# Kernel optimization log

Hardware: AMD Instinct MI355X
Metric: run time of the kernel (lower is better)

## Reference

```python
import jax, jax.numpy as jnp
import numpy as np

L, D, F, H = 4, 1024, 2048, 8
DH = D // H
EPS = 1e-5


def setup_inputs() -> dict:
    key = jax.random.key(0)
    ks = jax.random.split(key, 8)
    B, S = 4, 1024
    sd = 1.0 / np.sqrt(D)
    sf = 1.0 / np.sqrt(F)
    return {
        "X": jax.random.normal(ks[0], (B, S, D), jnp.float32),
        "Wq": jax.random.normal(ks[1], (L, D, D), jnp.float32) * sd,
        "Wk": jax.random.normal(ks[2], (L, D, D), jnp.float32) * sd,
        "Wv": jax.random.normal(ks[3], (L, D, D), jnp.float32) * sd,
        "Wg": jax.random.normal(ks[4], (L, D, D), jnp.float32) * sd,
        "Wo": jax.random.normal(ks[5], (L, D, D), jnp.float32) * sd,
        "W1": jax.random.normal(ks[6], (L, D, F), jnp.float32) * sd,
        "W2": jax.random.normal(ks[7], (L, F, D), jnp.float32) * sf,
        "ln_scale": jnp.ones((D,), jnp.float32),
        "ln_bias": jnp.zeros((D,), jnp.float32),
        "gn_scale": jnp.ones((L, D), jnp.float32),
        "gn_bias": jnp.zeros((L, D), jnp.float32),
    }


def _layer_norm(x, scale, bias):
    mu = x.mean(-1, keepdims=True)
    var = x.var(-1, keepdims=True)
    return (x - mu) * jax.lax.rsqrt(var + EPS) * scale + bias


def _rotate(x, cos, sin):
    # x: (B,S,H,DH); cos/sin: (1,S,1,DH//2); rotary pairs (even, odd)
    x1, x2 = x[..., 0::2], x[..., 1::2]
    r1 = x1 * cos - x2 * sin
    r2 = x1 * sin + x2 * cos
    return jnp.stack([r1, r2], axis=-1).reshape(x.shape)


def _decay_matrix(S):
    # D[h,n,m] = gamma_h^(n-m) for n>=m else 0
    gammas = 1.0 - jnp.exp(jnp.linspace(np.log(1 / 32), np.log(1 / 512), H)).astype(jnp.float32)
    n = jnp.arange(S)
    diff = (n[:, None] - n[None, :]).astype(jnp.float32)
    pw = jnp.exp(jnp.clip(diff, 0.0)[None] * jnp.log(gammas)[:, None, None])
    return jnp.where(diff[None] >= 0, pw, 0.0)  # (H,S,S)


def _retention(x, Wq, Wk, Wv, Wg, Wo, gn_s, gn_b, Dm, cos, sin):
    B, S, _ = x.shape
    Q = (x @ Wq).reshape(B, S, H, DH)
    K = (x @ Wk).reshape(B, S, H, DH)
    V = (x @ Wv).reshape(B, S, H, DH)
    Q = _rotate(Q, cos, sin)
    K = _rotate(K, cos, -sin)  # conjugate phase
    att = jnp.einsum('bnhd,bmhd->bhnm', Q, K) * Dm  # (B,H,S,S)
    Y = jnp.einsum('bhnm,bmhd->bnhd', att, V)
    # group norm: normalize each head's output per token
    mu = Y.mean(-1, keepdims=True)
    var = Y.var(-1, keepdims=True)
    Y = (Y - mu) * jax.lax.rsqrt(var + EPS)
    Y = Y.reshape(B, S, D) * gn_s + gn_b
    G = jax.nn.swish(x @ Wg)
    return (G * Y) @ Wo


def reference(X, Wq, Wk, Wv, Wg, Wo, W1, W2, ln_scale, ln_bias, gn_scale, gn_bias):
    B, S, _ = X.shape
    pos = jnp.arange(S, dtype=jnp.float32)
    inv_freq = 1.0 / (10000.0 ** (jnp.arange(0, DH, 2, dtype=jnp.float32) / DH))
    ang = pos[:, None] * inv_freq[None, :]  # (S, DH//2)
    cos = jnp.cos(ang)[None, :, None, :]
    sin = jnp.sin(ang)[None, :, None, :]
    Dm = _decay_matrix(S)
    for i in range(L):
        Yr = _retention(_layer_norm(X, ln_scale, ln_bias), Wq[i], Wk[i], Wv[i],
                        Wg[i], Wo[i], gn_scale[i], gn_bias[i], Dm, cos, sin) + X
        X = jax.nn.gelu(_layer_norm(Yr, ln_scale, ln_bias) @ W1[i]) @ W2[i] + Yr
    return X
```

## Files before the change

kernel.cpp:

```cpp
#include <hip/hip_runtime.h>
#include <hip/hip_bf16.h>
#include <cmath>

#define LAYERS 4
#define Bb 4
#define Ss 1024
#define Dd 1024
#define Ff 2048
#define Hh 8
#define DHd 128
#define Mm (Bb * Ss)
#define EPSf 1e-5f
#define LDQ 4096

typedef __attribute__((ext_vector_type(8))) short short8v;
typedef __attribute__((ext_vector_type(4))) float f32x4;
typedef __attribute__((ext_vector_type(4))) unsigned int u32x4;

__device__ __forceinline__ float swish_f(float x) { return x / (1.f + expf(-x)); }
__device__ __forceinline__ float gelu_f(float x) {
  return 0.5f * x * (1.f + tanhf(0.7978845608028654f * (x + 0.044715f * x * x * x)));
}
__device__ __forceinline__ unsigned short f2bfu(float f) {
  __hip_bfloat16 h = __float2bfloat16(f);
  return __builtin_bit_cast(unsigned short, h);
}
__device__ __forceinline__ float bfu2f(unsigned short u) {
  unsigned v = ((unsigned)u) << 16;
  return __builtin_bit_cast(float, v);
}
__device__ __forceinline__ void gl_lds16(const void* g, void* l) {
  __builtin_amdgcn_global_load_lds((__attribute__((address_space(1))) void*)g,
                                   (__attribute__((address_space(3))) void*)l, 16, 0, 0);
}
__device__ __forceinline__ f32x4 mfma16(short8v a, short8v b, f32x4 c) {
  return __builtin_amdgcn_mfma_f32_16x16x32_bf16(a, b, c, 0, 0, 0);
}

__global__ __launch_bounds__(256) void ln_bf16_kernel(const float* __restrict__ x,
                                                      short* __restrict__ outb,
                                                      const float* __restrict__ sc,
                                                      const float* __restrict__ bi) {
  const int row = blockIdx.x;
  const int t = threadIdx.x;
  const float4 v = *(const float4*)(x + (size_t)row * Dd + t * 4);
  float s = v.x + v.y + v.z + v.w;
  float s2 = v.x * v.x + v.y * v.y + v.z * v.z + v.w * v.w;
#pragma unroll
  for (int o = 32; o > 0; o >>= 1) { s += __shfl_down(s, o); s2 += __shfl_down(s2, o); }
  __shared__ float ps[4], ps2[4];
  if ((t & 63) == 0) { ps[t >> 6] = s; ps2[t >> 6] = s2; }
  __syncthreads();
  s = ps[0] + ps[1] + ps[2] + ps[3];
  s2 = ps2[0] + ps2[1] + ps2[2] + ps2[3];
  const float mu = s * (1.f / Dd);
  const float var = s2 * (1.f / Dd) - mu * mu;
  const float rstd = rsqrtf(var + EPSf);
  const float4 g = *(const float4*)(sc + t * 4);
  const float4 b = *(const float4*)(bi + t * 4);
  const float o0 = (v.x - mu) * rstd * g.x + b.x;
  const float o1 = (v.y - mu) * rstd * g.y + b.y;
  const float o2 = (v.z - mu) * rstd * g.z + b.z;
  const float o3 = (v.w - mu) * rstd * g.w + b.w;
  unsigned p0 = (unsigned)f2bfu(o0) | ((unsigned)f2bfu(o1) << 16);
  unsigned p1 = (unsigned)f2bfu(o2) | ((unsigned)f2bfu(o3) << 16);
  uint2 pk; pk.x = p0; pk.y = p1;
  *(uint2*)(outb + (size_t)row * Dd + t * 4) = pk;
}

__global__ void rope_table_kernel(float* __restrict__ ct, float* __restrict__ st) {
  const int i = blockIdx.x * 256 + threadIdx.x;
  const int s = i >> 6, f = i & 63;
  const float inv = powf(10000.f, -(float)f / 64.f);
  const float a = (float)s * inv;
  ct[i] = cosf(a);
  st[i] = sinf(a);
}

__global__ void rope_ip_kernel(short* __restrict__ QK, const float* __restrict__ ct,
                               const float* __restrict__ st) {
  const int idx = blockIdx.x * 256 + threadIdx.x;
  const int f = idx & 63;
  const int h = (idx >> 6) & 7;
  const int r = idx >> 9;
  const int s = r & (Ss - 1);
  const float c = ct[(s << 6) + f], sn = st[(s << 6) + f];
  const size_t qo = (size_t)r * LDQ + h * DHd + 2 * f;
  const unsigned qp = *(const unsigned*)(QK + qo);
  const unsigned kp = *(const unsigned*)(QK + qo + 1024);
  const float qx = bfu2f((unsigned short)(qp & 0xffff)), qy = bfu2f((unsigned short)(qp >> 16));
  const float kx = bfu2f((unsigned short)(kp & 0xffff)), ky = bfu2f((unsigned short)(kp >> 16));
  const unsigned qn = (unsigned)f2bfu(qx * c - qy * sn) | ((unsigned)f2bfu(qx * sn + qy * c) << 16);
  const unsigned kn = (unsigned)f2bfu(kx * c + ky * sn) | ((unsigned)f2bfu(-kx * sn + ky * c) << 16);
  *(unsigned*)(QK + qo) = qn;
  *(unsigned*)(QK + qo + 1024) = kn;
}

__global__ __launch_bounds__(256) void wtrans4_kernel(const float* __restrict__ W0,
                                                      const float* __restrict__ W1,
                                                      const float* __restrict__ W2,
                                                      const float* __restrict__ W3,
                                                      short* __restrict__ Wt) {
  __shared__ float tile[32][33];
  const int t = threadIdx.x;
  const int n0 = blockIdx.x * 32, k0 = blockIdx.y * 32;
  const int which = n0 >> 10;
  const float* W = (which == 0) ? W0 : (which == 1) ? W1 : (which == 2) ? W2 : W3;
  const int nl = n0 & 1023;
  const int tc = t & 31, tr8 = t >> 5;
#pragma unroll
  for (int i = 0; i < 4; ++i) {
    const int r = tr8 + i * 8;
    tile[r][tc] = W[(size_t)(k0 + r) * 1024 + nl + tc];
  }
  __syncthreads();
#pragma unroll
  for (int i = 0; i < 4; ++i) {
    const int r = tr8 + i * 8;
    Wt[(size_t)(n0 + r) * 1024 + k0 + tc] = (short)f2bfu(tile[tc][r]);
  }
}

__global__ __launch_bounds__(256) void wtrans1_kernel(const float* __restrict__ W,
                                                      short* __restrict__ Wt, int K, int N) {
  __shared__ float tile[32][33];
  const int t = threadIdx.x;
  const int n0 = blockIdx.x * 32, k0 = blockIdx.y * 32;
  const int tc = t & 31, tr8 = t >> 5;
#pragma unroll
  for (int i = 0; i < 4; ++i) {
    const int r = tr8 + i * 8;
    tile[r][tc] = W[(size_t)(k0 + r) * N + n0 + tc];
  }
  __syncthreads();
#pragma unroll
  for (int i = 0; i < 4; ++i) {
    const int r = tr8 + i * 8;
    Wt[(size_t)(n0 + r) * K + k0 + tc] = (short)f2bfu(tile[tc][r]);
  }
}

__global__ __launch_bounds__(256) void vtrans16_kernel(const short* __restrict__ Vb,
                                                       short* __restrict__ Vt) {
  __shared__ short tile[32][33];
  const int t = threadIdx.x;
  const int s0 = blockIdx.x * 32, d0 = blockIdx.y * 32, bh = blockIdx.z;
  const int bb = bh >> 3, h = bh & 7;
  const int tc = t & 31, tr8 = t >> 5;
#pragma unroll
  for (int i = 0; i < 4; ++i) {
    const int r = tr8 + i * 8;
    tile[r][tc] = Vb[(size_t)(bb * Ss + s0 + r) * LDQ + 2048 + h * DHd + d0 + tc];
  }
  __syncthreads();
#pragma unroll
  for (int i = 0; i < 4; ++i) {
    const int r = tr8 + i * 8;
    Vt[(size_t)(bh * DHd + d0 + r) * Ss + s0 + tc] = tile[tc][r];
  }
}

template <int EPI>
__global__ __launch_bounds__(512, 2) void gemm10(const short* __restrict__ A,
                                                 const short* __restrict__ Bt,
                                                 float* __restrict__ Cf,
                                                 short* __restrict__ Cb,
                                                 const float* __restrict__ Res,
                                                 int N, int K, int ldc) {
  __shared__ __align__(16) short As[2][2][128 * 64];
  __shared__ __align__(16) short Bs[2][2][128 * 64];
  const int t = threadIdx.x;
  const int w = t >> 6, l = t & 63;
  const int lq = l >> 4, lr = l & 15;
  const int wr = w >> 2, wc = w & 3;
  const int bhalf = wc >> 1, brow0 = (wc & 1) * 64;
  const int nwg = gridDim.x * gridDim.y;
  const int bid0 = blockIdx.x + blockIdx.y * gridDim.x;
  const int lgid = (bid0 & 7) * (nwg >> 3) + (bid0 >> 3);
  const int bx = lgid % gridDim.x, by = lgid / gridDim.x;
  const int row0 = by * 256, col0 = bx * 256;
  const int NT = K >> 6;

  f32x4 acc[8][4] = {};
  short8v a[4][2], b[4][2];

  auto stageA = [&](int kt, int hf) {
    const int db = kt & 1;
#pragma unroll
    for (int i = 0; i < 2; ++i) {
      const int c = t + i * 512;
      const int row = c >> 3, slot = c & 7;
      gl_lds16(A + (size_t)(row0 + hf * 128 + row) * K + kt * 64 + ((slot ^ (row & 7)) << 3),
               &As[db][hf][c * 8]);
    }
  };
  auto stageB = [&](int kt, int hf) {
    const int db = kt & 1;
#pragma unroll
    for (int i = 0; i < 2; ++i) {
      const int c = t + i * 512;
      const int row = c >> 3, slot = c & 7;
      gl_lds16(Bt + (size_t)(col0 + hf * 128 + row) * K + kt * 64 + ((slot ^ (row & 7)) << 3),
               &Bs[db][hf][c * 8]);
    }
  };
  auto rdA = [&](int db, int m, int ks) -> short8v {
    const int row = m * 16 + lr;
    return *(const short8v*)&As[db][wr][row * 64 + (((ks << 2) + lq) ^ (row & 7)) * 8];
  };
  auto rdB = [&](int db, int n, int ks) -> short8v {
    const int row = brow0 + n * 16 + lr;
    return *(const short8v*)&Bs[db][bhalf][row * 64 + (((ks << 2) + lq) ^ (row & 7)) * 8];
  };

  stageA(0, 0); stageA(0, 1); stageB(0, 0); stageB(0, 1);
  if (NT > 1) { stageB(1, 0); stageB(1, 1); }
  if (NT > 1) { asm volatile("s_waitcnt vmcnt(4)" ::: "memory"); }
  else        { asm volatile("s_waitcnt vmcnt(0)" ::: "memory"); }
  asm volatile("s_barrier" ::: "memory");

  for (int kt = 0; kt < NT; ++kt) {
    const int db = kt & 1;
#pragma unroll
    for (int m = 0; m < 4; ++m) { a[m][0] = rdA(db, m, 0); a[m][1] = rdA(db, m, 1); }
#pragma unroll
    for (int n = 0; n < 2; ++n) { b[n][0] = rdB(db, n, 0); b[n][1] = rdB(db, n, 1); }
    if (kt + 1 < NT) stageA(kt + 1, 0);
    __builtin_amdgcn_s_setprio(1);
#pragma unroll
    for (int m = 0; m < 4; ++m)
#pragma unroll
      for (int n = 0; n < 2; ++n) {
        acc[m][n] = mfma16(a[m][0], b[n][0], acc[m][n]);
        acc[m][n] = mfma16(a[m][1], b[n][1], acc[m][n]);
      }
    __builtin_amdgcn_s_setprio(0);
    asm volatile("s_barrier" ::: "memory");
#pragma unroll
    for (int n = 2; n < 4; ++n) { b[n][0] = rdB(db, n, 0); b[n][1] = rdB(db, n, 1); }
    if (kt + 1 < NT) stageA(kt + 1, 1);
    __builtin_amdgcn_s_setprio(1);
#pragma unroll
    for (int m = 0; m < 4; ++m)
#pragma unroll
      for (int n = 2; n < 4; ++n) {
        acc[m][n] = mfma16(a[m][0], b[n][0], acc[m][n]);
        acc[m][n] = mfma16(a[m][1], b[n][1], acc[m][n]);
      }
    __builtin_amdgcn_s_setprio(0);
    asm volatile("s_barrier" ::: "memory");
#pragma unroll
    for (int m = 0; m < 4; ++m) { a[m][0] = rdA(db, m + 4, 0); a[m][1] = rdA(db, m + 4, 1); }
    if (kt + 2 < NT) stageB(kt + 2, 0);
    __builtin_amdgcn_s_setprio(1);
#pragma unroll
    for (int m = 0; m < 4; ++m)
#pragma unroll
      for (int n = 0; n < 2; ++n) {
        acc[m + 4][n] = mfma16(a[m][0], b[n][0], acc[m + 4][n]);
        acc[m + 4][n] = mfma16(a[m][1], b[n][1], acc[m + 4][n]);
      }
    __builtin_amdgcn_s_setprio(0);
    asm volatile("s_barrier" ::: "memory");
    if (kt + 2 < NT) stageB(kt + 2, 1);
    __builtin_amdgcn_s_setprio(1);
#pragma unroll
    for (int m = 0; m < 4; ++m)
#pragma unroll
      for (int n = 2; n < 4; ++n) {
        acc[m + 4][n] = mfma16(a[m][0], b[n][0], acc[m + 4][n]);
        acc[m + 4][n] = mfma16(a[m][1], b[n][1], acc[m + 4][n]);
      }
    __builtin_amdgcn_s_setprio(0);
    if (kt + 2 < NT) { asm volatile("s_waitcnt vmcnt(4)" ::: "memory"); }
    else             { asm volatile("s_waitcnt vmcnt(0)" ::: "memory"); }
    asm volatile("s_barrier" ::: "memory");
  }

#pragma unroll
  for (int m = 0; m < 8; ++m) {
#pragma unroll
    for (int n = 0; n < 4; ++n) {
#pragma unroll
      for (int r = 0; r < 4; ++r) {
        const int row = row0 + wr * 128 + m * 16 + lq * 4 + r;
        const int col = col0 + wc * 64 + n * 16 + lr;
        const size_t o = (size_t)row * ldc + col;
        float v = acc[m][n][r];
        if (EPI == 0) Cb[o] = (short)f2bfu(v);
        else if (EPI == 1) Cf[o] = v + Res[o];
        else Cb[o] = (short)f2bfu(gelu_f(v));
      }
    }
  }
}

template <int BM, int BN, int EPI>
__global__ __launch_bounds__(256) void gemm7(const short* __restrict__ A,
                                             const short* __restrict__ Bt,
                                             float* __restrict__ Cf,
                                             short* __restrict__ Cb,
                                             const float* __restrict__ Res,
                                             int N, int K, int ldc) {
  constexpr int NTHR = 256;
  constexpr int WM = BM / 2, WN = BN / 2;
  constexpr int MR = WM / 16, NR = WN / 16;
  constexpr int LA = (BM * 4) / NTHR, LB = (BN * 4) / NTHR;
  __shared__ __align__(16) short As[2][BM * 32];
  __shared__ __align__(16) short Bs[2][BN * 32];
  const int t = threadIdx.x;
  const int w = t >> 6, l = t & 63;
  const int lq = l >> 4, lr = l & 15;
  const int wr = w >> 1, wc = w & 1;
  const int nwg = gridDim.x * gridDim.y;
  const int bid0 = blockIdx.x + blockIdx.y * gridDim.x;
  const int lgid = (bid0 & 7) * (nwg >> 3) + (bid0 >> 3);
  const int bx = lgid % gridDim.x, by = lgid / gridDim.x;
  const int row0 = by * BM, col0 = bx * BN;
  f32x4 acc[MR][NR] = {};
  const int NTK = K >> 5;

  auto stage = [&](int tile, int buf) {
    const int k0 = tile << 5;
#pragma unroll
    for (int i = 0; i < LA; ++i) {
      const int c = t + i * NTHR;
      const int row = c >> 2, sc = c & 3;
      gl_lds16(A + (size_t)(row0 + row) * K + k0 + ((sc ^ ((row >> 1) & 3)) << 3),
               &As[buf][c * 8]);
    }
#pragma unroll
    for (int i = 0; i < LB; ++i) {
      const int c = t + i * NTHR;
      const int row = c >> 2, sc = c & 3;
      gl_lds16(Bt + (size_t)(col0 + row) * K + k0 + ((sc ^ ((row >> 1) & 3)) << 3),
               &Bs[buf][c * 8]);
    }
  };

  stage(0, 0);
  int cur = 0;
  for (int tt = 0; tt < NTK; ++tt) {
    __syncthreads();
    if (tt + 1 < NTK) stage(tt + 1, cur ^ 1);
    short8v a[MR], b[NR];
#pragma unroll
    for (int m = 0; m < MR; ++m) {
      const int row = wr * WM + m * 16 + lr;
      a[m] = *(const short8v*)&As[cur][row * 32 + ((lq ^ ((row >> 1) & 3)) << 3)];
    }
#pragma unroll
    for (int n = 0; n < NR; ++n) {
      const int col = wc * WN + n * 16 + lr;
      b[n] = *(const short8v*)&Bs[cur][col * 32 + ((lq ^ ((col >> 1) & 3)) << 3)];
    }
    __builtin_amdgcn_s_setprio(1);
#pragma unroll
    for (int m = 0; m < MR; ++m)
#pragma unroll
      for (int n = 0; n < NR; ++n) acc[m][n] = mfma16(a[m], b[n], acc[m][n]);
    __builtin_amdgcn_s_setprio(0);
    cur ^= 1;
  }

#pragma unroll
  for (int m = 0; m < MR; ++m) {
#pragma unroll
    for (int n = 0; n < NR; ++n) {
#pragma unroll
      for (int r = 0; r < 4; ++r) {
        const int row = row0 + wr * WM + m * 16 + lq * 4 + r;
        const int col = col0 + wc * WN + n * 16 + lr;
        const size_t o = (size_t)row * ldc + col;
        float v = acc[m][n][r];
        if (EPI == 0) Cb[o] = (short)f2bfu(v);
        else if (EPI == 1) Cf[o] = v + Res[o];
        else Cb[o] = (short)f2bfu(gelu_f(v));
      }
    }
  }
}

__global__ __launch_bounds__(256) void ret4_kernel(const short* __restrict__ QKb,
                                                   const short* __restrict__ Vt,
                                                   float* __restrict__ Y0,
                                                   float* __restrict__ Y1) {
  __shared__ __align__(16) short Ks[2][64 * 128];
  __shared__ __align__(16) short Vs[2][128 * 64];
  const int t = threadIdx.x, w = t >> 6, l = t & 63;
  const int lq = l >> 4, lr = l & 15;
  const int u = blockIdx.x;
  const int lgid = (u & 7) * 64 + (u >> 3);
  const int half = lgid >> 8;
  const int rest = lgid & 255;
  const int bh = rest >> 3, j = rest & 7;
  const int qb = half ? j : 7 - j;
  const int b = bh >> 3, h = bh & 7;
  const int q0 = qb * 128;
  const float lstep = (logf(1.f / 512.f) - logf(1.f / 32.f)) * (1.f / 7.f);
  const float gamma = 1.f - expf(logf(1.f / 32.f) + (float)h * lstep);
  const float l2g = logf(gamma) * 1.44269504f;
  const short* Qp = QKb;
  const short* Kp = QKb + 1024;

  short8v qf[2][4];
#pragma unroll
  for (int qn = 0; qn < 2; ++qn)
#pragma unroll
    for (int ks = 0; ks < 4; ++ks)
      qf[qn][ks] = *(const short8v*)(Qp + (size_t)(b * Ss + q0 + w * 32 + qn * 16 + lr) * LDQ +
                                     h * DHd + ks * 32 + lq * 8);

  float cmf[4], csr[4];
#pragma unroll
  for (int mf = 0; mf < 4; ++mf) cmf[mf] = exp2f(l2g * (float)(-16 * mf));
#pragma unroll
  for (int r = 0; r < 4; ++r) csr[r] = exp2f(l2g * (float)(63 - 4 * lq - r));

  f32x4 yacc[2][8] = {};
  const int nt = 2 * qb + 2;
  const int sb = ((lq & 1) * 2) * 16 + lr;

  auto stageKV = [&](int m0, int buf) {
#pragma unroll
    for (int i = 0; i < 4; ++i) {
      const int c = (w * 4 + i) * 64 + l;
      const int row = c >> 4, slot = c & 15;
      gl_lds16(Kp + (size_t)(b * Ss + m0 + row) * LDQ + h * DHd + ((slot ^ (row & 7)) * 8),
               &Ks[buf][(w * 4 + i) * 512]);
    }
#pragma unroll
    for (int i = 0; i < 4; ++i) {
      const int c = (w * 4 + i) * 64 + l;
      const int row = c >> 3, slot = c & 7;
      gl_lds16(Vt + (size_t)(bh * DHd + row) * Ss + m0 + ((slot ^ (row & 7)) * 8),
               &Vs[buf][(w * 4 + i) * 512]);
    }
  };

  stageKV(half * 64, 0);
  __syncthreads();
  int cur = 0;
  for (int tt = half; tt < nt; tt += 2) {
    const int m0 = tt * 64;
    if (tt + 2 < nt) stageKV((tt + 2) * 64, cur ^ 1);

    f32x4 st[4][2] = {};
    __builtin_amdgcn_s_setprio(1);
#pragma unroll
    for (int mf = 0; mf < 4; ++mf) {
      const int row = mf * 16 + lr;
#pragma unroll
      for (int ks = 0; ks < 4; ++ks) {
        short8v kf = *(const short8v*)&Ks[cur][row * 128 + (((4 * ks + lq) ^ (row & 7)) * 8)];
        st[mf][0] = mfma16(kf, qf[0][ks], st[mf][0]);
        st[mf][1] = mfma16(kf, qf[1][ks], st[mf][1]);
      }
    }
    __builtin_amdgcn_s_setprio(0);
    float rs[2];
#pragma unroll
    for (int qn = 0; qn < 2; ++qn)
      rs[qn] = exp2f(l2g * (float)(q0 + w * 32 + qn * 16 + lr - m0 - 63));
#pragma unroll
    for (int mf = 0; mf < 4; ++mf)
#pragma unroll
      for (int qn = 0; qn < 2; ++qn)
#pragma unroll
        for (int r = 0; r < 4; ++r) {
          const int qg = q0 + w * 32 + qn * 16 + lr;
          const int kvg = m0 + mf * 16 + lq * 4 + r;
          const float wgt = (qg >= kvg) ? rs[qn] * cmf[mf] * csr[r] : 0.f;
          st[mf][qn][r] *= wgt;
        }
    unsigned pk[4][2][2];
#pragma unroll
    for (int mf = 0; mf < 4; ++mf)
#pragma unroll
      for (int qn = 0; qn < 2; ++qn)
#pragma unroll
        for (int p = 0; p < 2; ++p)
          pk[mf][qn][p] = (unsigned)f2bfu(st[mf][qn][2 * p]) |
                          ((unsigned)f2bfu(st[mf][qn][2 * p + 1]) << 16);
    short8v afr[2][2];
#pragma unroll
    for (int qn = 0; qn < 2; ++qn)
#pragma unroll
      for (int ks2 = 0; ks2 < 2; ++ks2) {
        u32x4 wd;
#pragma unroll
        for (int wj = 0; wj < 4; ++wj) {
          const int src = sb + (wj >> 1) * 16;
          const unsigned v0 = __shfl(pk[2 * ks2 + 0][qn][wj & 1], src);
          const unsigned v1 = __shfl(pk[2 * ks2 + 1][qn][wj & 1], src);
          wd[wj] = (lq >= 2) ? v1 : v0;
        }
        afr[qn][ks2] = __builtin_bit_cast(short8v, wd);
      }
    __builtin_amdgcn_s_setprio(1);
#pragma unroll
    for (int nd = 0; nd < 8; ++nd) {
      const int row = nd * 16 + lr;
#pragma unroll
      for (int ks2 = 0; ks2 < 2; ++ks2) {
        short8v vf = *(const short8v*)&Vs[cur][row * 64 + (((4 * ks2 + lq) ^ (row & 7)) * 8)];
        yacc[0][nd] = mfma16(afr[0][ks2], vf, yacc[0][nd]);
        yacc[1][nd] = mfma16(afr[1][ks2], vf, yacc[1][nd]);
      }
    }
    __builtin_amdgcn_s_setprio(0);
    __syncthreads();
    cur ^= 1;
  }
  float* Y = half ? Y1 : Y0;
#pragma unroll
  for (int qn = 0; qn < 2; ++qn)
#pragma unroll
    for (int r = 0; r < 4; ++r) {
      const int q = q0 + w * 32 + qn * 16 + lq * 4 + r;
#pragma unroll
      for (int nd = 0; nd < 8; ++nd)
        Y[(size_t)(b * Ss + q) * Dd + h * DHd + nd * 16 + lr] = yacc[qn][nd][r];
    }
}

__global__ __launch_bounds__(256) void gate_kernel(const float* __restrict__ Y0,
                                                   const float* __restrict__ Y1,
                                                   const short* __restrict__ Graw,
                                                   short* __restrict__ Gb,
                                                   const float* __restrict__ gs,
                                                   const float* __restrict__ gb) {
  const int lane = threadIdx.x & 63;
  const int rowh = blockIdx.x * 4 + (threadIdx.x >> 6);
  const int h = rowh & 7;
  const int row = rowh >> 3;
  const size_t ybase = (size_t)row * Dd + (size_t)h * DHd + lane * 2;
  float2 a = *(const float2*)(Y0 + ybase);
  const float2 c = *(const float2*)(Y1 + ybase);
  a.x += c.x; a.y += c.y;
  float s = a.x + a.y, s2 = a.x * a.x + a.y * a.y;
#pragma unroll
  for (int o = 32; o > 0; o >>= 1) { s += __shfl_down(s, o); s2 += __shfl_down(s2, o); }
  s = __shfl(s, 0);
  s2 = __shfl(s2, 0);
  const float mu = s * (1.f / DHd);
  const float rstd = rsqrtf(s2 * (1.f / DHd) - mu * mu + EPSf);
  const int d = h * DHd + lane * 2;
  const float2 g = *(const float2*)(gs + d);
  const float2 bbv = *(const float2*)(gb + d);
  const float y0 = (a.x - mu) * rstd * g.x + bbv.x;
  const float y1 = (a.y - mu) * rstd * g.y + bbv.y;
  const unsigned gr = *(const unsigned*)(Graw + (size_t)row * LDQ + 3072 + h * DHd + lane * 2);
  const float gx = bfu2f((unsigned short)(gr & 0xffff));
  const float gy = bfu2f((unsigned short)(gr >> 16));
  const unsigned o01 = (unsigned)f2bfu(swish_f(gx) * y0) |
                       ((unsigned)f2bfu(swish_f(gy) * y1) << 16);
  *(unsigned*)(Gb + ybase) = o01;
}

extern "C" void kernel_launch(void* const* d_in, const int* in_sizes, int n_in,
                              void* d_out, int out_size, void* d_ws, size_t ws_size,
                              hipStream_t stream) {
  const float* X = (const float*)d_in[0];
  const float* Wq = (const float*)d_in[1];
  const float* Wk = (const float*)d_in[2];
  const float* Wv = (const float*)d_in[3];
  const float* Wg = (const float*)d_in[4];
  const float* Wo = (const float*)d_in[5];
  const float* W1 = (const float*)d_in[6];
  const float* W2 = (const float*)d_in[7];
  const float* lns = (const float*)d_in[8];
  const float* lnb = (const float*)d_in[9];
  const float* gns = (const float*)d_in[10];
  const float* gnb = (const float*)d_in[11];
  float* out = (float*)d_out;

  char* W = (char*)d_ws;
  const size_t MB = 1u << 20;
  float* Abuf  = (float*)(W);
  short* Xnb   = (short*)(W + 16 * MB);
  short* QKVGb = (short*)(W + 24 * MB);
  float* Y0    = (float*)(W + 56 * MB);
  float* Y1    = (float*)(W + 72 * MB);
  short* Vtb   = (short*)(W + 88 * MB);
  short* Gb    = (short*)(W + 96 * MB);
  short* Wqkvgt= (short*)(W + 104 * MB);
  short* Wot   = (short*)(W + 112 * MB);
  short* W1t   = (short*)(W + 114 * MB);
  short* W2t   = (short*)(W + 118 * MB);
  float* ct    = (float*)(W + 122 * MB);
  float* st    = ct + Ss * 64;
  short* Hb = QKVGb;

  hipMemcpyAsync(Abuf, X, (size_t)Mm * Dd * sizeof(float), hipMemcpyDeviceToDevice, stream);
  rope_table_kernel<<<(Ss * 64) / 256, 256, 0, stream>>>(ct, st);

  for (int l = 0; l < LAYERS; ++l) {
    const size_t DD = (size_t)Dd * Dd;
    wtrans4_kernel<<<dim3(128, 32), 256, 0, stream>>>(Wq + l * DD, Wk + l * DD, Wv + l * DD,
                                                      Wg + l * DD, Wqkvgt);
    wtrans1_kernel<<<dim3(32, 32), 256, 0, stream>>>(Wo + l * DD, Wot, Dd, Dd);
    wtrans1_kernel<<<dim3(64, 32), 256, 0, stream>>>(W1 + (size_t)l * Dd * Ff, W1t, Dd, Ff);
    wtrans1_kernel<<<dim3(32, 64), 256, 0, stream>>>(W2 + (size_t)l * Ff * Dd, W2t, Ff, Dd);

    ln_bf16_kernel<<<Mm, 256, 0, stream>>>(Abuf, Xnb, lns, lnb);
    gemm10<0><<<dim3(16, 16), 512, 0, stream>>>(Xnb, Wqkvgt, nullptr, QKVGb,
                                                nullptr, 4096, Dd, LDQ);
    rope_ip_kernel<<<(Bb * Ss * Hh * 64) / 256, 256, 0, stream>>>(QKVGb, ct, st);
    vtrans16_kernel<<<dim3(Ss / 32, DHd / 32, Bb * Hh), 256, 0, stream>>>(QKVGb, Vtb);
    ret4_kernel<<<512, 256, 0, stream>>>(QKVGb, Vtb, Y0, Y1);
    gate_kernel<<<(Mm * Hh) / 4, 256, 0, stream>>>(Y0, Y1, QKVGb, Gb,
                                                   gns + (size_t)l * Dd, gnb + (size_t)l * Dd);
    gemm7<128, 64, 1><<<dim3(16, 32), 256, 0, stream>>>(Gb, Wot, Abuf, nullptr, Abuf,
                                                        Dd, Dd, Dd);
    ln_bf16_kernel<<<Mm, 256, 0, stream>>>(Abuf, Xnb, lns, lnb);
    gemm7<128, 64, 2><<<dim3(32, 32), 256, 0, stream>>>(Xnb, W1t, nullptr, Hb, nullptr,
                                                        Ff, Dd, Ff);
    float* dst = (l == LAYERS - 1) ? out : Abuf;
    gemm7<64, 64, 1><<<dim3(16, 64), 256, 0, stream>>>(Hb, W2t, dst, nullptr, Abuf,
                                                       Dd, Ff, Dd);
  }
}
```

Measured before the change: 826.1 us.

## Add 256x128 triple-buffered GEMM kernel for the FFN up-projection

Adds a new gemm11 kernel with 256x128 tiles, 512 threads, a three-stage LDS pipeline with split A staging, and a grouped workgroup-to-tile remapping. It replaces gemm7<128,64> for the W1 GEMM with fused GELU. The larger tile raises arithmetic intensity and reuse per block, and the remap is meant to improve L2 locality. In exchange the grid is only 256 workgroups, which could limit occupancy on a chip with many CUs, and LDS use is high (144KB).

```diff
diff --git a/kernel.cpp b/kernel.cpp
--- a/kernel.cpp
+++ b/kernel.cpp
@@ -285,6 +285,113 @@
       for (int r = 0; r < 4; ++r) {
         const int row = row0 + wr * 128 + m * 16 + lq * 4 + r;
         const int col = col0 + wc * 64 + n * 16 + lr;
+        const size_t o = (size_t)row * ldc + col;
+        float v = acc[m][n][r];
+        if (EPI == 0) Cb[o] = (short)f2bfu(v);
+        else if (EPI == 1) Cf[o] = v + Res[o];
+        else Cb[o] = (short)f2bfu(gelu_f(v));
+      }
+    }
+  }
+}
+
+template <int EPI>
+__global__ __launch_bounds__(512) void gemm11(const short* __restrict__ A,
+                                              const short* __restrict__ Bt,
+                                              float* __restrict__ Cf,
+                                              short* __restrict__ Cb,
+                                              const float* __restrict__ Res,
+                                              int K, int lda, int ldb, int ldc, int nxt) {
+  __shared__ __align__(16) short As[3][256 * 64];
+  __shared__ __align__(16) short Bs[3][128 * 64];
+  const int t = threadIdx.x;
+  const int w = t >> 6, l = t & 63;
+  const int lq = l >> 4, lr = l & 15;
+  const int wr = w >> 2, wc = w & 3;
+  const int nwg = gridDim.x;
+  const int lgid = (blockIdx.x & 7) * (nwg >> 3) + (blockIdx.x >> 3);
+  const int mt = lgid / nxt, nt_ = lgid % nxt;
+  const int row0 = mt * 256, col0 = nt_ * 128;
+  const int NT = K >> 6;
+  f32x4 acc[8][2] = {};
+  short8v a[4][2], b[2][2];
+
+  auto stageA = [&](int kt, int hf) {
+    const int s = kt % 3;
+#pragma unroll
+    for (int i = 0; i < 2; ++i) {
+      const int c = t + i * 512;
+      const int row = c >> 3, slot = c & 7;
+      gl_lds16(A + (size_t)(row0 + hf * 128 + row) * lda + kt * 64 + ((slot ^ (row & 7)) << 3),
+               &As[s][hf * 8192 + c * 8]);
+    }
+  };
+  auto stageB = [&](int kt) {
+    const int s = kt % 3;
+#pragma unroll
+    for (int i = 0; i < 2; ++i) {
+      const int c = t + i * 512;
+      const int row = c >> 3, slot = c & 7;
+      gl_lds16(Bt + (size_t)(col0 + row) * ldb + kt * 64 + ((slot ^ (row & 7)) << 3),
+               &Bs[s][c * 8]);
+    }
+  };
+  auto rdA = [&](int s, int m, int ks) -> short8v {
+    const int row = wr * 128 + m * 16 + lr;
+    return *(const short8v*)&As[s][row * 64 + (((ks << 2) + lq) ^ (row & 7)) * 8];
+  };
+  auto rdB = [&](int s, int n, int ks) -> short8v {
+    const int row = wc * 32 + n * 16 + lr;
+    return *(const short8v*)&Bs[s][row * 64 + (((ks << 2) + lq) ^ (row & 7)) * 8];
+  };
+
+  stageA(0, 0); stageA(0, 1); stageB(0);
+  stageA(1, 0); stageA(1, 1); stageB(1);
+  asm volatile("s_waitcnt vmcnt(6)" ::: "memory");
+  asm volatile("s_barrier" ::: "memory");
+
+  for (int kt = 0; kt < NT; ++kt) {
+    const int s = kt % 3;
+#pragma unroll
+    for (int m = 0; m < 4; ++m) { a[m][0] = rdA(s, m, 0); a[m][1] = rdA(s, m, 1); }
+#pragma unroll
+    for (int n = 0; n < 2; ++n) { b[n][0] = rdB(s, n, 0); b[n][1] = rdB(s, n, 1); }
+    if (kt + 2 < NT) stageA(kt + 2, 0);
+    __builtin_amdgcn_s_setprio(1);
+#pragma unroll
+    for (int m = 0; m < 4; ++m)
+#pragma unroll
+      for (int n = 0; n < 2; ++n) {
+        acc[m][n] = mfma16(a[m][0], b[n][0], acc[m][n]);
+        acc[m][n] = mfma16(a[m][1], b[n][1], acc[m][n]);
+      }
+    __builtin_amdgcn_s_setprio(0);
+    asm volatile("s_barrier" ::: "memory");
+#pragma unroll
+    for (int m = 0; m < 4; ++m) { a[m][0] = rdA(s, m + 4, 0); a[m][1] = rdA(s, m + 4, 1); }
+    if (kt + 2 < NT) { stageA(kt + 2, 1); stageB(kt + 2); }
+    __builtin_amdgcn_s_setprio(1);
+#pragma unroll
+    for (int m = 0; m < 4; ++m)
+#pragma unroll
+      for (int n = 0; n < 2; ++n) {
+        acc[m + 4][n] = mfma16(a[m][0], b[n][0], acc[m + 4][n]);
+        acc[m + 4][n] = mfma16(a[m][1], b[n][1], acc[m + 4][n]);
+      }
+    __builtin_amdgcn_s_setprio(0);
+    if (kt + 2 < NT) { asm volatile("s_waitcnt vmcnt(6)" ::: "memory"); }
+    else             { asm volatile("s_waitcnt vmcnt(0)" ::: "memory"); }
+    asm volatile("s_barrier" ::: "memory");
+  }
+
+#pragma unroll
+  for (int m = 0; m < 8; ++m) {
+#pragma unroll
+    for (int n = 0; n < 2; ++n) {
+#pragma unroll
+      for (int r = 0; r < 4; ++r) {
+        const int row = row0 + wr * 128 + m * 16 + lq * 4 + r;
+        const int col = col0 + wc * 32 + n * 16 + lr;
         const size_t o = (size_t)row * ldc + col;
         float v = acc[m][n][r];
         if (EPI == 0) Cb[o] = (short)f2bfu(v);
@@ -614,8 +721,8 @@
     gemm7<128, 64, 1><<<dim3(16, 32), 256, 0, stream>>>(Gb, Wot, Abuf, nullptr, Abuf,
                                                         Dd, Dd, Dd);
     ln_bf16_kernel<<<Mm, 256, 0, stream>>>(Abuf, Xnb, lns, lnb);
-    gemm7<128, 64, 2><<<dim3(32, 32), 256, 0, stream>>>(Xnb, W1t, nullptr, Hb, nullptr,
-                                                        Ff, Dd, Ff);
+    gemm11<2><<<256, 512, 0, stream>>>(Xnb, W1t, nullptr, Hb, nullptr,
+                                       Dd, Dd, Dd, Ff, 16);
     float* dst = (l == LAYERS - 1) ? out : Abuf;
     gemm7<64, 64, 1><<<dim3(16, 64), 256, 0, stream>>>(Hb, W2t, dst, nullptr, Abuf,
                                                        Dd, Ff, Dd);
```

Measured after the change: 801.2 us. -3.0%, faster.
